# Kernel tuning notes

Measured on AMD Instinct MI355X. Metric: run time of the kernel, lower is better.

The kernel has to match this reference:

```python
import jax, jax.numpy as jnp
import numpy as np

M_HIST = 6
LAM = 1e-4
THRESHOLD = 50
BETA = 1.0


def _f_step(z, x, Wh, bh, Wx, bx, Wo, bo):
    # DEQ cell: f(z, x) = tanh(Linear(tanh(h_layer(x) + x_layer(z))))
    # (note: Func.forward(x, z) is called as f(z, x), so h_layer sees the
    #  external input x and x_layer sees the iterate z)
    hidden = jnp.tanh(x @ Wh.T + bh + z @ Wx.T + bx)  # [B,S,H]
    return jnp.tanh(hidden @ Wo.T + bo)               # [B,S,D]


def _anderson(f, x0):
    bsz = x0.shape[0]
    dL = x0.shape[1] * x0.shape[2]
    flat = lambda z: z.reshape(bsz, dL)
    unflat = lambda z: z.reshape(x0.shape)

    X = jnp.zeros((bsz, M_HIST, dL), dtype=x0.dtype)
    F = jnp.zeros((bsz, M_HIST, dL), dtype=x0.dtype)
    F0 = flat(f(x0))
    X = X.at[:, 0].set(flat(x0))
    F = F.at[:, 0].set(F0)
    X = X.at[:, 1].set(F0)
    F = F.at[:, 1].set(flat(f(unflat(F0))))

    lowest = jnp.asarray(1e8, dtype=x0.dtype)
    lowest_x = jnp.zeros((bsz, dL), dtype=x0.dtype)

    for k in range(2, THRESHOLD):  # fixed unrolled solver iterations
        n = min(k, M_HIST)
        G = F[:, :n] - X[:, :n]                       # [B,n,dL]
        GG = jnp.einsum('bnd,bmd->bnm', G, G) + LAM * jnp.eye(n, dtype=x0.dtype)
        H = jnp.zeros((bsz, n + 1, n + 1), dtype=x0.dtype)
        H = H.at[:, 0, 1:].set(1.0)
        H = H.at[:, 1:, 0].set(1.0)
        H = H.at[:, 1:, 1:].set(GG)
        rhs = jnp.zeros((bsz, n + 1, 1), dtype=x0.dtype).at[:, 0, 0].set(1.0)
        alpha = jnp.linalg.solve(H, rhs)[:, 1:, 0]    # [B,n]
        Xk = BETA * jnp.einsum('bn,bnd->bd', alpha, F[:, :n]) \
            + (1.0 - BETA) * jnp.einsum('bn,bnd->bd', alpha, X[:, :n])
        Fk = flat(f(unflat(Xk)))
        X = X.at[:, k % M_HIST].set(Xk)
        F = F.at[:, k % M_HIST].set(Fk)
        abs_diff = jnp.linalg.norm(Fk - Xk)
        rel_diff = abs_diff / (1e-5 + jnp.linalg.norm(Fk))
        better = rel_diff < lowest
        lowest_x = jnp.where(better, Xk, lowest_x)
        lowest = jnp.minimum(rel_diff, lowest)
    return unflat(lowest_x)


def setup_inputs() -> dict:
    key = jax.random.key(0)
    ks = jax.random.split(key, 9)
    B, S, D, H, O = 16384, 31, 14, 50, 1
    sc = lambda fan_in: 1.0 / np.sqrt(fan_in)
    return {
        'x':  jax.random.normal(ks[0], (B, S, D), jnp.float32),
        'Wh': jax.random.normal(ks[1], (H, D), jnp.float32) * sc(D),
        'bh': jax.random.normal(ks[2], (H,), jnp.float32) * sc(D),
        'Wx': jax.random.normal(ks[3], (H, D), jnp.float32) * sc(D),
        'bx': jax.random.normal(ks[4], (H,), jnp.float32) * sc(D),
        'Wo': jax.random.normal(ks[5], (D, H), jnp.float32) * sc(H),
        'bo': jax.random.normal(ks[6], (D,), jnp.float32) * sc(H),
        'Wf': jax.random.normal(ks[7], (O, S * D), jnp.float32) * sc(S * D),
        'bf': jax.random.normal(ks[8], (O,), jnp.float32) * sc(S * D),
    }


def reference(x, Wh, bh, Wx, bx, Wo, bo, Wf, bf):
    f = lambda z: _f_step(z, x, Wh, bh, Wx, bx, Wo, bo)
    z_star = _anderson(f, jnp.zeros_like(x))   # fixed-point solve (no grad)
    z = f(z_star)                              # one extra f application
    out = z.reshape(z.shape[0], -1) @ Wf.T + bf  # [B,1]
    return out
```

## Files before the change

### kernel.cpp

```cpp
#include <hip/hip_runtime.h>
#include <hip/hip_fp16.h>

#define S 31
#define D 14
#define H 50
#define NB 16384
#define NITER 48
#define LAMR 1e-4f

#define WS_D2   0
#define WS_F2   64
#define WS_WHP  128
#define WS_BHX  928
#define WS_BO   992
#define WS_WX2  1024
#define WS_WO2  1424
#define WS_WF2  1792
#define WS_OUTK 4096

typedef _Float16 f16x2 __attribute__((ext_vector_type(2)));

#if defined(__has_builtin) && __has_builtin(__builtin_amdgcn_rcpf)
#define FRCP(x) __builtin_amdgcn_rcpf(x)
#else
#define FRCP(x) (1.0f/(x))
#endif

#define FDOT2(a,b,c) __builtin_amdgcn_fdot2((a),(b),(c),false)

__device__ __forceinline__ f16x2 pkrtz(float a, float b){
  auto r = __builtin_amdgcn_cvt_pkrtz(a, b);
  return __builtin_bit_cast(f16x2, r);
}
#define PKRTZ(a,b) pkrtz((a),(b))

#define AIJ(i,j) ((i)*6 - ((i)*((i)+1))/2 + (j))

__device__ __forceinline__ float tfast(float x){
  float e = __expf(x + x);
  return 1.f - 2.f * FRCP(e + 1.f);
}

__device__ __forceinline__ float half_red(float v){
  v += __shfl_xor(v, 1);
  v += __shfl_xor(v, 2);
  v += __shfl_xor(v, 4);
  v += __shfl_xor(v, 8);
  v += __shfl_xor(v, 16);
  return v;
}

__global__ void prep_kernel(const float* __restrict__ Wh, const float* __restrict__ bh,
                            const float* __restrict__ Wx, const float* __restrict__ bx,
                            const float* __restrict__ Wo, const float* __restrict__ bo,
                            const float* __restrict__ Wf, float* __restrict__ ws){
  int t = threadIdx.x;
  for (int i=t;i<128;i+=256) ws[i]=0.f;
  for (int i=t;i<800;i+=256){
    int h=i>>4, d=i&15;
    ws[WS_WHP+i] = (d<D)? Wh[h*D+d] : 0.f;
  }
  for (int i=t;i<64;i+=256) ws[WS_BHX+i] = (i<H)? bh[i]+bx[i] : 0.f;
  for (int i=t;i<16;i+=256) ws[WS_BO+i]  = (i<D)? bo[i] : 0.f;
  __half2* wx2 = (__half2*)(ws + WS_WX2);
  for (int i=t;i<400;i+=256){
    int h=i>>3, dd=i&7, d0=2*dd, d1=2*dd+1;
    float a=(d0<D)?Wx[h*D+d0]:0.f, b=(d1<D)?Wx[h*D+d1]:0.f;
    wx2[i] = __floats2half2_rn(a,b);
  }
  __half2* wo2 = (__half2*)(ws + WS_WO2);
  for (int i=t;i<364;i+=256){
    int d=i/26, hh=i-26*d, h0=2*hh, h1=2*hh+1;
    float a=(hh<25)?Wo[d*H+h0]:0.f, b=(hh<25)?Wo[d*H+h1]:0.f;
    wo2[i] = __floats2half2_rn(a,b);
  }
  __half2* wf2 = (__half2*)(ws + WS_WF2);
  for (int i=t;i<256;i+=256){
    int s=i>>3, dd=i&7, d0=2*dd, d1=2*dd+1;
    float a=(s<S && d0<D)?Wf[s*D+d0]:0.f, b=(s<S && d1<D)?Wf[s*D+d1]:0.f;
    wf2[i] = __floats2half2_rn(a,b);
  }
}

#define FEVAL() do{ \
  f16x2 thh[25]; \
  _Pragma("unroll") \
  for (int hh_=0; hh_<25; ++hh_){ \
    float a0_ = hxr[2*hh_], b0_ = hxr[2*hh_+1]; \
    _Pragma("unroll") for (int q_=0;q_<7;++q_){ \
      a0_ = FDOT2(xvh[q_], wx2[(2*hh_)*8+q_],   a0_); \
      b0_ = FDOT2(xvh[q_], wx2[(2*hh_+1)*8+q_], b0_); } \
    thh[hh_] = PKRTZ(tfast(a0_), tfast(b0_)); \
  } \
  _Pragma("unroll") \
  for (int dp_=0; dp_<7; ++dp_){ \
    float t0_ = bop[2*dp_], t1_ = bop[2*dp_+1]; \
    float t0b_ = 0.f, t1b_ = 0.f; \
    _Pragma("unroll") for (int hh_=0;hh_<25;hh_+=2){ \
      t0_ = FDOT2(thh[hh_], wo2[(2*dp_)*26+hh_],   t0_); \
      t1_ = FDOT2(thh[hh_], wo2[(2*dp_+1)*26+hh_], t1_); } \
    _Pragma("unroll") for (int hh_=1;hh_<25;hh_+=2){ \
      t0b_ = FDOT2(thh[hh_], wo2[(2*dp_)*26+hh_],   t0b_); \
      t1b_ = FDOT2(thh[hh_], wo2[(2*dp_+1)*26+hh_], t1b_); } \
    fvh[dp_] = PKRTZ(tfast(t0_+t0b_), tfast(t1_+t1b_)); \
  } \
}while(0)

#define ZERO_INACT() do{ \
  if (!act){ \
    _Pragma("unroll") for (int q_=0;q_<7;++q_){ fvh[q_]=zzv; gvh[q_]=zzv; } \
  } \
}while(0)

#define PUSH() do{ \
  float dnew_[5]; \
  _Pragma("unroll") for (int j_=0;j_<5;++j_){ \
    float acc_=0.f; \
    _Pragma("unroll") for (int q_=0;q_<7;++q_) acc_ = FDOT2(gvh[q_], Gh[(j_+1)*7+q_], acc_); \
    dnew_[j_] = half_red(acc_); } \
  d2l=0.f; f2l=0.f; \
  _Pragma("unroll") for (int q_=0;q_<7;++q_){ \
    d2l = FDOT2(gvh[q_], gvh[q_], d2l); \
    f2l = FDOT2(fvh[q_], fvh[q_], f2l); } \
  d2r = half_red(d2l); f2r = half_red(f2l); \
  _Pragma("unroll") for (int j_=0;j_<5;++j_) \
    _Pragma("unroll") for (int q_=0;q_<7;++q_){ \
      Fh[j_*7+q_] = Fh[(j_+1)*7+q_]; Gh[j_*7+q_] = Gh[(j_+1)*7+q_]; } \
  _Pragma("unroll") for (int q_=0;q_<7;++q_){ Fh[35+q_]=fvh[q_]; Gh[35+q_]=gvh[q_]; } \
  _Pragma("unroll") for (int i_=0;i_<5;++i_) \
    _Pragma("unroll") for (int j_=i_;j_<5;++j_) GG[AIJ(i_,j_)] = GG[AIJ(i_+1,j_+1)]; \
  _Pragma("unroll") for (int j_=0;j_<5;++j_) GG[AIJ(j_,5)] = dnew_[j_]; \
  GG[AIJ(5,5)] = d2r; \
}while(0)

__global__ __launch_bounds__(256, 3)
void solver_kernel(const float* __restrict__ x,
                   const float* __restrict__ whp, const float* __restrict__ bhx,
                   const float* __restrict__ bop,
                   const f16x2* __restrict__ wx2, const f16x2* __restrict__ wo2,
                   const f16x2* __restrict__ wf2,
                   float* __restrict__ outk, float* __restrict__ d2p, float* __restrict__ f2p){
  const int tid  = threadIdx.x;
  const int lane = tid & 63;
  const int s    = tid & 31;
  const int elem = blockIdx.x*8 + (tid>>5);
  const bool act = (s < S);

  __shared__ float hx_sh[256*51];
  float* hxw = hx_sh + tid*51;

  {
    float xd[D];
#pragma unroll
    for (int d=0; d<D; ++d) xd[d]=0.f;
    if (act){
      const float* xr = x + ((size_t)elem*S + s)*D;
#pragma unroll
      for (int d=0; d<D; ++d) xd[d]=xr[d];
    }
#pragma unroll 2
    for (int h=0; h<H; ++h){
      float a0 = bhx[h], a1 = 0.f;
#pragma unroll
      for (int d=0; d<D; d+=2){ a0 += xd[d]*whp[h*16+d]; a1 += xd[d+1]*whp[h*16+d+1]; }
      hxw[h] = a0+a1;
    }
  }
  const float* hxr = hxw;
  const f16x2 zzv = {(_Float16)0.f, (_Float16)0.f};

  f16x2 Fh[42], Gh[42], xvh[7], fvh[7], gvh[7];
  float GG[21];
  float d2l, f2l, d2r, f2r;
#pragma unroll
  for (int i=0;i<42;++i){ Fh[i]=zzv; Gh[i]=zzv; }
#pragma unroll
  for (int i=0;i<21;++i) GG[i]=0.f;

#pragma unroll
  for (int q=0;q<7;++q) xvh[q]=zzv;
  FEVAL();
#pragma unroll
  for (int q=0;q<7;++q) gvh[q]=fvh[q]-xvh[q];
  ZERO_INACT();
  PUSH();
#pragma unroll
  for (int q=0;q<7;++q) xvh[q]=fvh[q];
  FEVAL();
#pragma unroll
  for (int q=0;q<7;++q) gvh[q]=fvh[q]-xvh[q];
  ZERO_INACT();
  PUSH();

#pragma unroll 1
  for (int kk=2; kk<50; ++kk){
    float A_[21], invd[6], yv[6];
    if (kk >= 6){
#pragma unroll
      for (int i=0;i<6;++i)
#pragma unroll
        for (int j=i;j<6;++j) A_[AIJ(i,j)] = GG[AIJ(i,j)] + ((i==j)?LAMR:0.f);
    } else {
      int lo = 6-kk;
#pragma unroll
      for (int i=0;i<6;++i)
#pragma unroll
        for (int j=i;j<6;++j){
          float v = GG[AIJ(i,j)] + ((i==j)?LAMR:0.f);
          A_[AIJ(i,j)] = (i>=lo)? v : ((i==j)?1e30f:0.f);
        }
    }
#pragma unroll
    for (int i=0;i<6;++i) yv[i]=1.f;
#pragma unroll
    for (int p=0;p<6;++p){
      invd[p] = FRCP(A_[AIJ(p,p)]);
#pragma unroll
      for (int i=p+1;i<6;++i){
        float m = A_[AIJ(p,i)]*invd[p];
#pragma unroll
        for (int j=i;j<6;++j) A_[AIJ(i,j)] -= m*A_[AIJ(p,j)];
        yv[i] -= m*yv[p];
      }
    }
#pragma unroll
    for (int p=5;p>=0;--p){
      float acc=yv[p];
#pragma unroll
      for (int j=p+1;j<6;++j) acc -= A_[AIJ(p,j)]*yv[j];
      yv[p]=acc*invd[p];
    }
    float isum = FRCP(yv[0]+yv[1]+yv[2]+yv[3]+yv[4]+yv[5]);
#pragma unroll
    for (int q=0;q<7;++q) xvh[q]=zzv;
#pragma unroll
    for (int j=0;j<6;++j){
      _Float16 ah = (_Float16)(yv[j]*isum);
      f16x2 a2 = {ah, ah};
#pragma unroll
      for (int q=0;q<7;++q) xvh[q] += a2*Fh[j*7+q];
    }
    FEVAL();
#pragma unroll
    for (int q=0;q<7;++q) gvh[q]=fvh[q]-xvh[q];
    ZERO_INACT();
    PUSH();
    float po=0.f;
    const f16x2* wfr = wf2 + s*8;
#pragma unroll
    for (int q=0;q<7;++q) po = FDOT2(fvh[q], wfr[q], po);
    po = half_red(po);
    float d2w = d2r + __shfl_xor(d2r, 32);
    float f2w = f2r + __shfl_xor(f2r, 32);
    if (lane==0){ atomicAdd(&d2p[kk-2], d2w); atomicAdd(&f2p[kk-2], f2w); }
    if (s==0) outk[(size_t)(kk-2)*NB + elem] = po;
  }
}

__global__ void final_kernel(const float* __restrict__ d2p, const float* __restrict__ f2p,
                             const float* __restrict__ outk, const float* __restrict__ bf,
                             float* __restrict__ out){
  int b = blockIdx.x*blockDim.x + threadIdx.x;
  float best = 1e8f; int kst = 0;
  for (int k=0;k<NITER;++k){
    float rel = sqrtf(d2p[k]) / (1e-5f + sqrtf(f2p[k]));
    if (rel < best){ best = rel; kst = k; }
  }
  out[b] = outk[(size_t)kst*NB + b] + bf[0];
}

extern "C" void kernel_launch(void* const* d_in, const int* in_sizes, int n_in,
                              void* d_out, int out_size, void* d_ws, size_t ws_size,
                              hipStream_t stream){
  const float* x  = (const float*)d_in[0];
  const float* Wh = (const float*)d_in[1];
  const float* bh = (const float*)d_in[2];
  const float* Wx = (const float*)d_in[3];
  const float* bx = (const float*)d_in[4];
  const float* Wo = (const float*)d_in[5];
  const float* bo = (const float*)d_in[6];
  const float* Wf = (const float*)d_in[7];
  const float* bf = (const float*)d_in[8];
  float* ws  = (float*)d_ws;
  float* out = (float*)d_out;

  hipLaunchKernelGGL(prep_kernel, dim3(1), dim3(256), 0, stream, Wh,bh,Wx,bx,Wo,bo,Wf,ws);
  hipLaunchKernelGGL(solver_kernel, dim3(NB/8), dim3(256), 0, stream,
                     x, ws+WS_WHP, ws+WS_BHX, ws+WS_BO,
                     (const f16x2*)(ws+WS_WX2), (const f16x2*)(ws+WS_WO2), (const f16x2*)(ws+WS_WF2),
                     ws+WS_OUTK, ws+WS_D2, ws+WS_F2);
  hipLaunchKernelGGL(final_kernel, dim3(NB/256), dim3(256), 0, stream,
                     ws+WS_D2, ws+WS_F2, ws+WS_OUTK, bf, out);
}
```

Before: 3.247 ms.

## Use circular history slots, fuse FEVAL output accumulation, store hx in fp16

The Anderson history now uses a circular slot index with a switch-dispatched write, replacing the per-iteration register shift of Fh/Gh/GG. The two prologue evaluations are folded into the main loop. FEVAL accumulates the output layer inside the hidden loop, so the 25-entry hidden array no longer has to stay live. The per-thread hx precompute is stored in shared memory as packed fp16, roughly halving its LDS footprint, and tanh now calls exp2 directly with a prescaled argument. The goal is to cut register moves and pressure and raise occupancy, at the cost of lower hx precision and possible register spilling from the switch dispatch.

```diff
diff --git a/kernel.cpp b/kernel.cpp
--- a/kernel.cpp
+++ b/kernel.cpp
@@ -26,6 +26,12 @@
 #define FRCP(x) (1.0f/(x))
 #endif
 
+#if defined(__has_builtin) && __has_builtin(__builtin_amdgcn_exp2f)
+#define FEXP2(x) __builtin_amdgcn_exp2f(x)
+#else
+#define FEXP2(x) exp2f(x)
+#endif
+
 #define FDOT2(a,b,c) __builtin_amdgcn_fdot2((a),(b),(c),false)
 
 __device__ __forceinline__ f16x2 pkrtz(float a, float b){
@@ -34,10 +40,15 @@
 }
 #define PKRTZ(a,b) pkrtz((a),(b))
 
+__device__ __forceinline__ f16x2 pack_rn(float a, float b){
+  __half2 h = __floats2half2_rn(a, b);
+  return __builtin_bit_cast(f16x2, h);
+}
+
 #define AIJ(i,j) ((i)*6 - ((i)*((i)+1))/2 + (j))
 
 __device__ __forceinline__ float tfast(float x){
-  float e = __expf(x + x);
+  float e = FEXP2(x * 2.8853900817779268f);
   return 1.f - 2.f * FRCP(e + 1.f);
 }
 
@@ -83,27 +94,21 @@
 }
 
 #define FEVAL() do{ \
-  f16x2 thh[25]; \
+  float oacc_[14]; \
+  _Pragma("unroll") for (int d_=0; d_<14; ++d_) oacc_[d_] = bop[d_]; \
   _Pragma("unroll") \
   for (int hh_=0; hh_<25; ++hh_){ \
-    float a0_ = hxr[2*hh_], b0_ = hxr[2*hh_+1]; \
+    f16x2 hx2_ = hxr2[hh_]; \
+    float a0_ = (float)hx2_[0], b0_ = (float)hx2_[1]; \
     _Pragma("unroll") for (int q_=0;q_<7;++q_){ \
       a0_ = FDOT2(xvh[q_], wx2[(2*hh_)*8+q_],   a0_); \
       b0_ = FDOT2(xvh[q_], wx2[(2*hh_+1)*8+q_], b0_); } \
-    thh[hh_] = PKRTZ(tfast(a0_), tfast(b0_)); \
+    f16x2 th_ = PKRTZ(tfast(a0_), tfast(b0_)); \
+    _Pragma("unroll") for (int d_=0; d_<14; ++d_) \
+      oacc_[d_] = FDOT2(th_, wo2[d_*26+hh_], oacc_[d_]); \
   } \
-  _Pragma("unroll") \
-  for (int dp_=0; dp_<7; ++dp_){ \
-    float t0_ = bop[2*dp_], t1_ = bop[2*dp_+1]; \
-    float t0b_ = 0.f, t1b_ = 0.f; \
-    _Pragma("unroll") for (int hh_=0;hh_<25;hh_+=2){ \
-      t0_ = FDOT2(thh[hh_], wo2[(2*dp_)*26+hh_],   t0_); \
-      t1_ = FDOT2(thh[hh_], wo2[(2*dp_+1)*26+hh_], t1_); } \
-    _Pragma("unroll") for (int hh_=1;hh_<25;hh_+=2){ \
-      t0b_ = FDOT2(thh[hh_], wo2[(2*dp_)*26+hh_],   t0b_); \
-      t1b_ = FDOT2(thh[hh_], wo2[(2*dp_+1)*26+hh_], t1b_); } \
-    fvh[dp_] = PKRTZ(tfast(t0_+t0b_), tfast(t1_+t1b_)); \
-  } \
+  _Pragma("unroll") for (int dp_=0; dp_<7; ++dp_) \
+    fvh[dp_] = PKRTZ(tfast(oacc_[2*dp_]), tfast(oacc_[2*dp_+1])); \
 }while(0)
 
 #define ZERO_INACT() do{ \
@@ -112,25 +117,31 @@
   } \
 }while(0)
 
-#define PUSH() do{ \
-  float dnew_[5]; \
-  _Pragma("unroll") for (int j_=0;j_<5;++j_){ \
+#define PUSH_SLOT(C) do{ \
+  _Pragma("unroll") for (int q_=0;q_<7;++q_){ Fh[(C)*7+q_]=fvh[q_]; Gh[(C)*7+q_]=gvh[q_]; } \
+  _Pragma("unroll") for (int j_=0;j_<6;++j_){ \
+    if (j_ != (C)) GG[ (j_<(C)) ? AIJ(j_,(C)) : AIJ((C),j_) ] = dnr_[j_]; } \
+  GG[AIJ((C),(C))] = d2r; \
+}while(0)
+
+#define PUSH(SLOT_) do{ \
+  float dnr_[6]; \
+  _Pragma("unroll") for (int j_=0;j_<6;++j_){ \
     float acc_=0.f; \
-    _Pragma("unroll") for (int q_=0;q_<7;++q_) acc_ = FDOT2(gvh[q_], Gh[(j_+1)*7+q_], acc_); \
-    dnew_[j_] = half_red(acc_); } \
+    _Pragma("unroll") for (int q_=0;q_<7;++q_) acc_ = FDOT2(gvh[q_], Gh[j_*7+q_], acc_); \
+    dnr_[j_] = half_red(acc_); } \
   d2l=0.f; f2l=0.f; \
   _Pragma("unroll") for (int q_=0;q_<7;++q_){ \
     d2l = FDOT2(gvh[q_], gvh[q_], d2l); \
     f2l = FDOT2(fvh[q_], fvh[q_], f2l); } \
   d2r = half_red(d2l); f2r = half_red(f2l); \
-  _Pragma("unroll") for (int j_=0;j_<5;++j_) \
-    _Pragma("unroll") for (int q_=0;q_<7;++q_){ \
-      Fh[j_*7+q_] = Fh[(j_+1)*7+q_]; Gh[j_*7+q_] = Gh[(j_+1)*7+q_]; } \
-  _Pragma("unroll") for (int q_=0;q_<7;++q_){ Fh[35+q_]=fvh[q_]; Gh[35+q_]=gvh[q_]; } \
-  _Pragma("unroll") for (int i_=0;i_<5;++i_) \
-    _Pragma("unroll") for (int j_=i_;j_<5;++j_) GG[AIJ(i_,j_)] = GG[AIJ(i_+1,j_+1)]; \
-  _Pragma("unroll") for (int j_=0;j_<5;++j_) GG[AIJ(j_,5)] = dnew_[j_]; \
-  GG[AIJ(5,5)] = d2r; \
+  switch(SLOT_){ \
+    case 0: PUSH_SLOT(0); break; \
+    case 1: PUSH_SLOT(1); break; \
+    case 2: PUSH_SLOT(2); break; \
+    case 3: PUSH_SLOT(3); break; \
+    case 4: PUSH_SLOT(4); break; \
+    default: PUSH_SLOT(5); break; } \
 }while(0)
 
 __global__ __launch_bounds__(256, 3)
@@ -146,8 +157,8 @@
   const int elem = blockIdx.x*8 + (tid>>5);
   const bool act = (s < S);
 
-  __shared__ float hx_sh[256*51];
-  float* hxw = hx_sh + tid*51;
+  __shared__ f16x2 hx2_sh[256*27];
+  f16x2* hxw2 = hx2_sh + tid*27;
 
   {
     float xd[D];
@@ -158,15 +169,18 @@
 #pragma unroll
       for (int d=0; d<D; ++d) xd[d]=xr[d];
     }
-#pragma unroll 2
-    for (int h=0; h<H; ++h){
-      float a0 = bhx[h], a1 = 0.f;
-#pragma unroll
-      for (int d=0; d<D; d+=2){ a0 += xd[d]*whp[h*16+d]; a1 += xd[d+1]*whp[h*16+d+1]; }
-      hxw[h] = a0+a1;
+#pragma unroll 5
+    for (int hp=0; hp<25; ++hp){
+      float a0 = bhx[2*hp], a1 = bhx[2*hp+1];
+#pragma unroll
+      for (int d=0; d<D; ++d){
+        a0 += xd[d]*whp[(2*hp)*16+d];
+        a1 += xd[d]*whp[(2*hp+1)*16+d];
+      }
+      hxw2[hp] = pack_rn(a0, a1);
     }
   }
-  const float* hxr = hxw;
+  const f16x2* hxr2 = hxw2;
   const f16x2 zzv = {(_Float16)0.f, (_Float16)0.f};
 
   f16x2 Fh[42], Gh[42], xvh[7], fvh[7], gvh[7];
@@ -177,83 +191,79 @@
 #pragma unroll
   for (int i=0;i<21;++i) GG[i]=0.f;
 
-#pragma unroll
-  for (int q=0;q<7;++q) xvh[q]=zzv;
-  FEVAL();
-#pragma unroll
-  for (int q=0;q<7;++q) gvh[q]=fvh[q]-xvh[q];
-  ZERO_INACT();
-  PUSH();
-#pragma unroll
-  for (int q=0;q<7;++q) xvh[q]=fvh[q];
-  FEVAL();
-#pragma unroll
-  for (int q=0;q<7;++q) gvh[q]=fvh[q]-xvh[q];
-  ZERO_INACT();
-  PUSH();
-
+  int slot = 0;
 #pragma unroll 1
-  for (int kk=2; kk<50; ++kk){
-    float A_[21], invd[6], yv[6];
-    if (kk >= 6){
-#pragma unroll
-      for (int i=0;i<6;++i)
-#pragma unroll
-        for (int j=i;j<6;++j) A_[AIJ(i,j)] = GG[AIJ(i,j)] + ((i==j)?LAMR:0.f);
+  for (int kk=0; kk<50; ++kk){
+    if (kk == 0){
+#pragma unroll
+      for (int q=0;q<7;++q) xvh[q]=zzv;
+    } else if (kk == 1){
+#pragma unroll
+      for (int q=0;q<7;++q) xvh[q]=fvh[q];
     } else {
-      int lo = 6-kk;
-#pragma unroll
-      for (int i=0;i<6;++i)
-#pragma unroll
-        for (int j=i;j<6;++j){
-          float v = GG[AIJ(i,j)] + ((i==j)?LAMR:0.f);
-          A_[AIJ(i,j)] = (i>=lo)? v : ((i==j)?1e30f:0.f);
+      float A_[21], invd[6], yv[6];
+      if (kk >= 6){
+#pragma unroll
+        for (int i=0;i<6;++i)
+#pragma unroll
+          for (int j=i;j<6;++j) A_[AIJ(i,j)] = GG[AIJ(i,j)] + ((i==j)?LAMR:0.f);
+      } else {
+#pragma unroll
+        for (int i=0;i<6;++i)
+#pragma unroll
+          for (int j=i;j<6;++j){
+            float v = GG[AIJ(i,j)] + ((i==j)?LAMR:0.f);
+            A_[AIJ(i,j)] = (j < kk)? v : ((i==j)?1e30f:0.f);
+          }
+      }
+#pragma unroll
+      for (int i=0;i<6;++i) yv[i]=1.f;
+#pragma unroll
+      for (int p=0;p<6;++p){
+        invd[p] = FRCP(A_[AIJ(p,p)]);
+#pragma unroll
+        for (int i=p+1;i<6;++i){
+          float m = A_[AIJ(p,i)]*invd[p];
+#pragma unroll
+          for (int j=i;j<6;++j) A_[AIJ(i,j)] -= m*A_[AIJ(p,j)];
+          yv[i] -= m*yv[p];
         }
-    }
-#pragma unroll
-    for (int i=0;i<6;++i) yv[i]=1.f;
-#pragma unroll
-    for (int p=0;p<6;++p){
-      invd[p] = FRCP(A_[AIJ(p,p)]);
-#pragma unroll
-      for (int i=p+1;i<6;++i){
-        float m = A_[AIJ(p,i)]*invd[p];
-#pragma unroll
-        for (int j=i;j<6;++j) A_[AIJ(i,j)] -= m*A_[AIJ(p,j)];
-        yv[i] -= m*yv[p];
-      }
-    }
-#pragma unroll
-    for (int p=5;p>=0;--p){
-      float acc=yv[p];
-#pragma unroll
-      for (int j=p+1;j<6;++j) acc -= A_[AIJ(p,j)]*yv[j];
-      yv[p]=acc*invd[p];
-    }
-    float isum = FRCP(yv[0]+yv[1]+yv[2]+yv[3]+yv[4]+yv[5]);
-#pragma unroll
-    for (int q=0;q<7;++q) xvh[q]=zzv;
-#pragma unroll
-    for (int j=0;j<6;++j){
-      _Float16 ah = (_Float16)(yv[j]*isum);
-      f16x2 a2 = {ah, ah};
-#pragma unroll
-      for (int q=0;q<7;++q) xvh[q] += a2*Fh[j*7+q];
+      }
+#pragma unroll
+      for (int p=5;p>=0;--p){
+        float acc=yv[p];
+#pragma unroll
+        for (int j=p+1;j<6;++j) acc -= A_[AIJ(p,j)]*yv[j];
+        yv[p]=acc*invd[p];
+      }
+      float isum = FRCP(yv[0]+yv[1]+yv[2]+yv[3]+yv[4]+yv[5]);
+#pragma unroll
+      for (int q=0;q<7;++q) xvh[q]=zzv;
+#pragma unroll
+      for (int j=0;j<6;++j){
+        _Float16 ah = (_Float16)(yv[j]*isum);
+        f16x2 a2 = {ah, ah};
+#pragma unroll
+        for (int q=0;q<7;++q) xvh[q] += a2*Fh[j*7+q];
+      }
     }
     FEVAL();
 #pragma unroll
     for (int q=0;q<7;++q) gvh[q]=fvh[q]-xvh[q];
     ZERO_INACT();
-    PUSH();
-    float po=0.f;
-    const f16x2* wfr = wf2 + s*8;
-#pragma unroll
-    for (int q=0;q<7;++q) po = FDOT2(fvh[q], wfr[q], po);
-    po = half_red(po);
-    float d2w = d2r + __shfl_xor(d2r, 32);
-    float f2w = f2r + __shfl_xor(f2r, 32);
-    if (lane==0){ atomicAdd(&d2p[kk-2], d2w); atomicAdd(&f2p[kk-2], f2w); }
-    if (s==0) outk[(size_t)(kk-2)*NB + elem] = po;
+    PUSH(slot);
+    if (kk >= 2){
+      float po=0.f;
+      const f16x2* wfr = wf2 + s*8;
+#pragma unroll
+      for (int q=0;q<7;++q) po = FDOT2(fvh[q], wfr[q], po);
+      po = half_red(po);
+      float d2w = d2r + __shfl_xor(d2r, 32);
+      float f2w = f2r + __shfl_xor(f2r, 32);
+      if (lane==0){ atomicAdd(&d2p[kk-2], d2w); atomicAdd(&f2p[kk-2], f2w); }
+      if (s==0) outk[(size_t)(kk-2)*NB + elem] = po;
+    }
+    slot = (slot==5)? 0 : slot+1;
   }
 }
 
```

Result: slower. 5.270 ms (+62.3%).
